# Performance work log

Measured on AMD Instinct MI355X. Metric: run time of the kernel, lower is better.

Reference implementation:

```python
import jax, jax.numpy as jnp
import numpy as np

G = 32          # num graphs
NPG = 512       # nodes per graph
EPG = 4096      # edges per graph
DN = 128        # node/edge feat dim
DP = 64         # node identifier dim d_p
DE_ID = 64      # type identifier dim d_e
H = 768         # hidden_dim
IN_DIM = DN + 2 * DP + DE_ID  # 320


def setup_inputs() -> dict:
    key = jax.random.key(0)
    ks = jax.random.split(key, 9)
    N = G * NPG
    E = G * EPG
    x = jax.random.normal(ks[0], (N, DN), jnp.float32)
    edge_attr = jax.random.normal(ks[1], (E, DN), jnp.float32)
    P = jax.random.normal(ks[2], (N, DP), jnp.float32)  # ORF node identifiers
    E_V = jax.random.normal(ks[3], (1, DE_ID), jnp.float32) * 0.1
    E_E = jax.random.normal(ks[4], (1, DE_ID), jnp.float32) * 0.1
    W = jax.random.normal(ks[5], (H, IN_DIM), jnp.float32) / np.sqrt(IN_DIM)
    b = jnp.zeros((H,), jnp.float32)
    graph_token = jax.random.normal(ks[6], (1, H), jnp.float32) * 0.1
    # edges stay within their graph and are sorted by graph id
    base = jnp.repeat(jnp.arange(G, dtype=jnp.int32) * NPG, EPG)  # [E]
    src = base + jax.random.randint(ks[7], (E,), 0, NPG, jnp.int32)
    dst = base + jax.random.randint(ks[8], (E,), 0, NPG, jnp.int32)
    edge_index = jnp.stack([src, dst], axis=0)  # [2, E]
    batch = jnp.repeat(jnp.arange(G, dtype=jnp.int32), NPG)  # [N]
    return {
        "x": x, "edge_attr": edge_attr, "P": P,
        "E_V": E_V, "E_E": E_E, "W": W, "b": b, "graph_token": graph_token,
        "edge_index": edge_index, "batch": batch,
        "num_graphs": G, "max_node_num": NPG, "max_edge_num": EPG,
    }


def reference(x, edge_attr, P, E_V, E_E, W, b, graph_token,
              edge_index, batch, num_graphs, max_node_num, max_edge_num):
    N = x.shape[0]
    E = edge_index.shape[1]
    Hd = W.shape[0]
    d_e = E_V.shape[1]

    # node tokens: [x | P | P | E_V] @ W^T + b
    X_v = jnp.concatenate([x, P, P, jnp.broadcast_to(E_V, (N, d_e))], axis=1)
    X_v_proj = X_v @ W.T + b  # [N, H]

    # edge tokens: [edge_attr | P_u | P_v | E_E] @ W^T + b
    P_u = P[edge_index[0]]
    P_v = P[edge_index[1]]
    X_e = jnp.concatenate([edge_attr, P_u, P_v, jnp.broadcast_to(E_E, (E, d_e))], axis=1)
    X_e_proj = X_e @ W.T + b  # [E, H]

    # ragged -> padded packing (replaces per-graph python loop)
    ones_n = jnp.ones((N,), jnp.int32)
    node_num = jax.ops.segment_sum(ones_n, batch, num_segments=num_graphs)  # [G]
    node_ptr = jnp.cumsum(node_num) - node_num  # exclusive prefix sum
    node_pos = jnp.arange(N, dtype=jnp.int32) - node_ptr[batch]  # position within graph

    edge_batch = batch[edge_index[0]]  # [E]
    ones_e = jnp.ones((E,), jnp.int32)
    edge_num = jax.ops.segment_sum(ones_e, edge_batch, num_segments=num_graphs)
    edge_ptr = jnp.cumsum(edge_num) - edge_num
    edge_pos = jnp.arange(E, dtype=jnp.int32) - edge_ptr[edge_batch]

    seq_len = 1 + max_node_num + max_edge_num  # +1 for [graph] token
    tokens = jnp.zeros((num_graphs, seq_len, Hd), X_v_proj.dtype)
    tokens = tokens.at[:, 0, :].set(graph_token[0])
    tokens = tokens.at[batch, 1 + node_pos].set(X_v_proj)
    tokens = tokens.at[edge_batch, 1 + max_node_num + edge_pos].set(X_e_proj)

    attention_masks = jnp.zeros((num_graphs, seq_len), bool)
    attention_masks = attention_masks.at[:, 0].set(True)
    attention_masks = attention_masks.at[batch, 1 + node_pos].set(True)
    attention_masks = attention_masks.at[edge_batch, 1 + max_node_num + edge_pos].set(True)

    return tokens, attention_masks
```

## Files before the change

### kernel.cpp

```cpp
#include <hip/hip_runtime.h>
#include <stdint.h>

#define NG   32
#define NPG  512
#define EPG  4096
#define DN   128
#define DP   64
#define NN   (NG*NPG)
#define NE   (NG*EPG)
#define KD   320
#define HD   768
#define SEQ  (1+NPG+EPG)
#define TOK_ELEMS ((size_t)NG*SEQ*HD)
#define MASK_ELEMS ((size_t)NG*SEQ)

typedef unsigned short u16;
typedef __attribute__((ext_vector_type(8))) __bf16 bf16x8;
typedef __attribute__((ext_vector_type(8))) short  s16x8;
typedef __attribute__((ext_vector_type(4))) float  f32x4;

__device__ __forceinline__ u16 f2bf(float f) {
    uint32_t u = __builtin_bit_cast(uint32_t, f);
    u += 0x7fffu + ((u >> 16) & 1u);
    return (u16)(u >> 16);
}

__device__ __forceinline__ int b_off(int row, int kb) {
    return ((row >> 1) << 7) + ((row & 1) << 6) + (kb ^ (((row >> 1) & 3) << 4));
}

__global__ void ptr_k(const int* __restrict__ batch, const int* __restrict__ eidx,
                      int* __restrict__ nptr, int* __restrict__ eptr) {
    int t = threadIdx.x;
    if (t < NG) {
        int g = t, lo = 0, hi = NN;
        while (lo < hi) { int mid = (lo + hi) >> 1; if (batch[mid] < g) lo = mid + 1; else hi = mid; }
        nptr[g] = lo;
    } else if (t < 2 * NG) {
        int g = t - NG, lo = 0, hi = NE;
        while (lo < hi) { int mid = (lo + hi) >> 1; if (batch[eidx[mid]] < g) lo = mid + 1; else hi = mid; }
        eptr[g] = lo;
    }
}

__global__ void wconv_k(const float* __restrict__ W, u16* __restrict__ Wb) {
    int i = blockIdx.x * 256 + threadIdx.x;
    if (i < KD * HD) Wb[i] = f2bf(W[i]);
}

__global__ void aux_k(const float* __restrict__ gt, float* __restrict__ out) {
    size_t i = (size_t)blockIdx.x * 256 + threadIdx.x;
    if (i < (size_t)NG * HD) {
        int g = (int)(i / HD), c = (int)(i % HD);
        out[(size_t)g * SEQ * HD + c] = gt[c];
    } else {
        size_t m = i - (size_t)NG * HD;
        if (m < MASK_ELEMS) out[TOK_ELEMS + m] = 1.0f;
    }
}

__global__ __launch_bounds__(256, 2)
void gemm_scatter(const float* __restrict__ x,  const float* __restrict__ ea,
                  const float* __restrict__ P,  const float* __restrict__ EV,
                  const float* __restrict__ EEv,const float* __restrict__ bias,
                  const int* __restrict__ eidx, const int* __restrict__ batch,
                  const u16* __restrict__ Wb,   const int* __restrict__ nptr,
                  const int* __restrict__ eptr, float* __restrict__ out)
{
    __shared__ __align__(16) char b_lds[2][8192];
    __shared__ int info_src[128], info_pu[128], info_pv[128], info_orow[128];

    const int tid  = threadIdx.x;
    const int lane = tid & 63;
    const int wid  = tid >> 6;
    const int lrow = lane & 15;
    const int lq   = lane >> 4;

    uint32_t g_off[2], l_off[2];
    #pragma unroll
    for (int i = 0; i < 2; ++i) {
        uint32_t u = (uint32_t)(i * 256 + tid);
        uint32_t row = u >> 3, c = u & 7;
        g_off[i] = row * (KD * 2) + c * 16;
        l_off[i] = ((c >> 2) * 4096u) + (uint32_t)b_off((int)row, (int)((c & 3) * 16));
    }
    const char* WbB = (const char*)Wb;

    const int r0  = blockIdx.x * 128;
    const bool isNode = (r0 < NN);
    const float* feat = isNode ? x  : ea;
    const float* idv  = isNode ? EV : EEv;

    if (tid < 128) {
        int r = r0 + tid;
        if (isNode) {
            int g = batch[r];
            info_src[tid] = r; info_pu[tid] = r; info_pv[tid] = r;
            info_orow[tid] = g * SEQ + 1 + (r - nptr[g]);
        } else {
            int e = r - NN;
            int s = eidx[e], d = eidx[NE + e];
            int g = batch[s];
            info_src[tid] = e; info_pu[tid] = s; info_pv[tid] = d;
            info_orow[tid] = g * SEQ + 1 + NPG + (e - eptr[g]);
        }
    }
    __syncthreads();

    bf16x8 afr[2][10];
    int obase[2][4];
    #pragma unroll
    for (int rb = 0; rb < 2; ++rb) {
        const int arow = wid * 32 + rb * 16 + lrow;
        const int fsrc = info_src[arow];
        const int pu   = info_pu[arow];
        const int pv   = info_pv[arow];
        #pragma unroll
        for (int s = 0; s < 10; ++s) {
            const int kg = s * 32 + lq * 8;
            const float* sp;
            if      (s < 4) sp = feat + (size_t)fsrc * DN + kg;
            else if (s < 6) sp = P + (size_t)pu * DP + (kg - DN);
            else if (s < 8) sp = P + (size_t)pv * DP + (kg - DN - DP);
            else            sp = idv + (kg - DN - 2 * DP);
            f32x4 f0 = *reinterpret_cast<const f32x4*>(sp);
            f32x4 f1 = *reinterpret_cast<const f32x4*>(sp + 4);
            s16x8 v;
            v[0]=(short)f2bf(f0[0]); v[1]=(short)f2bf(f0[1]);
            v[2]=(short)f2bf(f0[2]); v[3]=(short)f2bf(f0[3]);
            v[4]=(short)f2bf(f1[0]); v[5]=(short)f2bf(f1[1]);
            v[6]=(short)f2bf(f1[2]); v[7]=(short)f2bf(f1[3]);
            afr[rb][s] = __builtin_bit_cast(bf16x8, v);
        }
        #pragma unroll
        for (int j = 0; j < 4; ++j)
            obase[rb][j] = info_orow[wid * 32 + rb * 16 + lq * 4 + j] * HD;
    }

    const int roff = b_off(lrow, lq * 16);

    s16x8 pre[2];
    #pragma unroll
    for (int i = 0; i < 2; ++i)
        pre[i] = *reinterpret_cast<const s16x8*>(WbB + g_off[i]);

    int cur = 0;
    int nxt = 1;

    constexpr int S0[5] = {0, 7, 14, 20, 26};
    constexpr int S1[5] = {7, 14, 20, 26, 32};

    auto do_nt = [&](f32x4 (&acc)[2][4], float (&bv)[4],
                     f32x4 (&accP)[2][4], float (&bvP)[4],
                     int n0, int pn0) {
        #pragma unroll
        for (int rb = 0; rb < 2; ++rb)
            #pragma unroll
            for (int i = 0; i < 4; ++i) acc[rb][i] = (f32x4)0.f;
        #pragma unroll
        for (int ni = 0; ni < 4; ++ni)
            bv[ni] = bias[n0 + ni * 16 + lrow];

        #pragma unroll
        for (int kp = 0; kp < 5; ++kp) {
            cur ^= 1;
            char* bb = &b_lds[0][0] + cur * 8192;
            #pragma unroll
            for (int i = 0; i < 2; ++i)
                *reinterpret_cast<s16x8*>(bb + l_off[i]) = pre[i];
            {
                int tn  = (nxt < 60) ? nxt : 59; ++nxt;
                int ntn = tn / 5, kpn = tn - ntn * 5;
                const char* gb = WbB + (size_t)ntn * (64 * KD * 2) + kpn * 128;
                #pragma unroll
                for (int i = 0; i < 2; ++i)
                    pre[i] = *reinterpret_cast<const s16x8*>(gb + g_off[i]);
            }
            asm volatile("s_waitcnt lgkmcnt(0)" ::: "memory");
            __builtin_amdgcn_sched_barrier(0);
            __builtin_amdgcn_s_barrier();
            #pragma unroll
            for (int kk = 0; kk < 2; ++kk) {
                const int kt = kp * 2 + kk;
                const char* bs = bb + kk * 4096;
                #pragma unroll
                for (int ni = 0; ni < 4; ++ni) {
                    bf16x8 bf = *reinterpret_cast<const bf16x8*>(bs + ni * 1024 + roff);
                    acc[0][ni] = __builtin_amdgcn_mfma_f32_16x16x32_bf16(afr[0][kt], bf, acc[0][ni], 0, 0, 0);
                    acc[1][ni] = __builtin_amdgcn_mfma_f32_16x16x32_bf16(afr[1][kt], bf, acc[1][ni], 0, 0, 0);
                }
            }
            if (pn0 >= 0) {
                #pragma unroll
                for (int si = S0[kp]; si < S1[kp]; ++si) {
                    const int j  = si & 3;
                    const int rb = (si >> 2) & 1;
                    const int ni = si >> 3;
                    out[(size_t)(obase[rb][j] + pn0 + ni * 16 + lrow)] =
                        accP[rb][ni][j] + bvP[ni];
                }
            }
        }
    };

    f32x4 accA[2][4], accB[2][4];
    float bvA[4], bvB[4];
    #pragma unroll
    for (int p = 0; p < 6; ++p) {
        do_nt(accA, bvA, accB, bvB, (2 * p) * 64,     2 * p * 64 - 64);
        do_nt(accB, bvB, accA, bvA, (2 * p + 1) * 64, (2 * p + 1) * 64 - 64);
    }
    #pragma unroll
    for (int si = 0; si < 32; ++si) {
        const int j  = si & 3;
        const int rb = (si >> 2) & 1;
        const int ni = si >> 3;
        out[(size_t)(obase[rb][j] + 704 + ni * 16 + lrow)] = accB[rb][ni][j] + bvB[ni];
    }
}

extern "C" void kernel_launch(void* const* d_in, const int* in_sizes, int n_in,
                              void* d_out, int out_size, void* d_ws, size_t ws_size,
                              hipStream_t stream) {
    const float* x    = (const float*)d_in[0];
    const float* ea   = (const float*)d_in[1];
    const float* P    = (const float*)d_in[2];
    const float* EV   = (const float*)d_in[3];
    const float* EEv  = (const float*)d_in[4];
    const float* W    = (const float*)d_in[5];
    const float* bias = (const float*)d_in[6];
    const float* gt   = (const float*)d_in[7];
    const int* eidx   = (const int*)d_in[8];
    const int* batch  = (const int*)d_in[9];

    float* out = (float*)d_out;
    u16* Wb  = (u16*)d_ws;
    int* ints = (int*)((char*)d_ws + (size_t)KD * HD * 2);
    int *nptr = ints, *eptr = ints + 32;

    ptr_k<<<1, 64, 0, stream>>>(batch, eidx, nptr, eptr);
    wconv_k<<<(KD * HD + 255) / 256, 256, 0, stream>>>(W, Wb);
    aux_k<<<(int)(((size_t)NG * HD + MASK_ELEMS + 255) / 256), 256, 0, stream>>>(gt, out);
    gemm_scatter<<<dim3((NN + NE) / 128), 256, 0, stream>>>(
        x, ea, P, EV, EEv, bias, eidx, batch, Wb, nptr, eptr, out);
}
```

Measured before the change: 169.0 us.

## Drop double-buffered accumulator store interleave and raise occupancy to 3 blocks

Removes the ping-pong scheme in which the previous N-tile's results were stored while the next tile's MFMAs ran. Each tile now computes its accumulators and stores them right after, and the launch bound asks for 3 blocks per CU. The aim is to halve accumulator register pressure so more waves fit, and let the extra waves hide store latency instead of explicit software overlap. The cost is losing the in-block overlap of stores with compute, and possible spills under the tighter register budget.

```diff
diff --git a/kernel.cpp b/kernel.cpp
--- a/kernel.cpp
+++ b/kernel.cpp
@@ -59,7 +59,7 @@
     }
 }
 
-__global__ __launch_bounds__(256, 2)
+__global__ __launch_bounds__(256, 3)
 void gemm_scatter(const float* __restrict__ x,  const float* __restrict__ ea,
                   const float* __restrict__ P,  const float* __restrict__ EV,
                   const float* __restrict__ EEv,const float* __restrict__ bias,
@@ -146,20 +146,13 @@
 
     int cur = 0;
     int nxt = 1;
-
-    constexpr int S0[5] = {0, 7, 14, 20, 26};
-    constexpr int S1[5] = {7, 14, 20, 26, 32};
-
-    auto do_nt = [&](f32x4 (&acc)[2][4], float (&bv)[4],
-                     f32x4 (&accP)[2][4], float (&bvP)[4],
-                     int n0, int pn0) {
+    for (int nt = 0; nt < 12; ++nt) {
+        const int n0 = nt * 64;
+        f32x4 acc[2][4];
         #pragma unroll
         for (int rb = 0; rb < 2; ++rb)
             #pragma unroll
             for (int i = 0; i < 4; ++i) acc[rb][i] = (f32x4)0.f;
-        #pragma unroll
-        for (int ni = 0; ni < 4; ++ni)
-            bv[ni] = bias[n0 + ni * 16 + lrow];
 
         #pragma unroll
         for (int kp = 0; kp < 5; ++kp) {
@@ -190,32 +183,18 @@
                     acc[1][ni] = __builtin_amdgcn_mfma_f32_16x16x32_bf16(afr[1][kt], bf, acc[1][ni], 0, 0, 0);
                 }
             }
-            if (pn0 >= 0) {
+        }
+
+        #pragma unroll
+        for (int ni = 0; ni < 4; ++ni) {
+            float bv = bias[n0 + ni * 16 + lrow];
+            #pragma unroll
+            for (int rb = 0; rb < 2; ++rb)
                 #pragma unroll
-                for (int si = S0[kp]; si < S1[kp]; ++si) {
-                    const int j  = si & 3;
-                    const int rb = (si >> 2) & 1;
-                    const int ni = si >> 3;
-                    out[(size_t)(obase[rb][j] + pn0 + ni * 16 + lrow)] =
-                        accP[rb][ni][j] + bvP[ni];
-                }
-            }
-        }
-    };
-
-    f32x4 accA[2][4], accB[2][4];
-    float bvA[4], bvB[4];
-    #pragma unroll
-    for (int p = 0; p < 6; ++p) {
-        do_nt(accA, bvA, accB, bvB, (2 * p) * 64,     2 * p * 64 - 64);
-        do_nt(accB, bvB, accA, bvA, (2 * p + 1) * 64, (2 * p + 1) * 64 - 64);
-    }
-    #pragma unroll
-    for (int si = 0; si < 32; ++si) {
-        const int j  = si & 3;
-        const int rb = (si >> 2) & 1;
-        const int ni = si >> 3;
-        out[(size_t)(obase[rb][j] + 704 + ni * 16 + lrow)] = accB[rb][ni][j] + bvB[ni];
+                for (int j = 0; j < 4; ++j)
+                    out[(size_t)(obase[rb][j] + n0 + ni * 16 + lrow)] =
+                        acc[rb][ni][j] + bv;
+        }
     }
 }
 
```

Result: slower. 173.2 us (+2.5%).
